# Optimization experiments

Hardware: AMD Instinct MI355X
Metric: run time of the kernel (lower is better)

## Reference

```python
import jax, jax.numpy as jnp
import numpy as np

# dims: batch, tokens, model dim, heads, head_dim, context len, n_blocks, ffn dim
B, L, D, H, HD, S, NB, DFF = 1, 3072, 1024, 16, 64, 512, 2, 4096
T3, H3, W3 = 12, 16, 16  # latent video grid, T3*H3*W3 == L


def _ln(x):
    # LayerNorm, elementwise_affine=False, eps=1e-6
    m = jnp.mean(x, axis=-1, keepdims=True)
    v = jnp.mean(jnp.square(x - m), axis=-1, keepdims=True)
    return (x - m) * jax.lax.rsqrt(v + 1e-6)


def _rot_half(x):
    x1, x2 = jnp.split(x, 2, axis=-1)
    return jnp.concatenate([-x2, x1], axis=-1)


def _rope3d(head_dim, t, h, w):
    d = head_dim // 6
    def band(n):
        freqs = 1.0 / 10000.0 ** (np.arange(0, 2 * d, 2, dtype=np.float32) / (2 * d))
        return np.outer(np.arange(n, dtype=np.float32), freqs)  # [n, d]
    te, he, we = band(t), band(h), band(w)
    rope = np.zeros((t, h, w, head_dim), dtype=np.float32)
    rope[:, :, :, :d] = te[:, None, None, :]
    rope[:, :, :, d:2 * d] = he[None, :, None, :]
    rope[:, :, :, 2 * d:3 * d] = we[None, None, :, :]
    return jnp.asarray(rope.reshape(t * h * w, head_dim))


def _forward(x, timestep_emb, context_emb, rope_emb, adaW, adab, sqW, skW, svW,
             soW, sob, cqW, ckW, cvW, coW, cob, f1W, f1b, f2W, f2b):
    Bv, Lv, Dv = x.shape
    hd = rope_emb.shape[-1]
    nh = Dv // hd
    scale = hd ** -0.5
    cos = jnp.cos(rope_emb)[None, None]  # [1,1,L,hd]
    sin = jnp.sin(rope_emb)[None, None]

    def heads(y):  # [B,N,D] -> [B,H,N,hd]
        return y.reshape(Bv, -1, nh, hd).transpose(0, 2, 1, 3)

    def merge(y):  # [B,H,L,hd] -> [B,L,D]
        return y.transpose(0, 2, 1, 3).reshape(Bv, Lv, Dv)

    for i in range(adaW.shape[0]):
        mods = timestep_emb @ adaW[i].T + adab[i]  # [B, 6D]
        sh_msa, sc_msa, g_msa, sh_mlp, sc_mlp, g_mlp = jnp.split(mods, 6, axis=-1)
        # --- AdaLN + self-attention with RoPE ---
        hx = _ln(x) * (1.0 + sc_msa[:, None, :]) + sh_msa[:, None, :]
        q, k, v = heads(hx @ sqW[i].T), heads(hx @ skW[i].T), heads(hx @ svW[i].T)
        q = q * cos + _rot_half(q) * sin
        k = k * cos + _rot_half(k) * sin
        a = jax.nn.softmax(jnp.einsum('bhld,bhmd->bhlm', q, k) * scale, axis=-1)
        o = merge(jnp.einsum('bhlm,bhmd->bhld', a, v))
        x = x + g_msa[:, None, :] * (o @ soW[i].T + sob[i])
        # --- cross-attention (no gate, no modulation) ---
        hx = _ln(x)
        q = heads(hx @ cqW[i].T)
        k = heads(context_emb @ ckW[i].T)
        v = heads(context_emb @ cvW[i].T)
        a = jax.nn.softmax(jnp.einsum('bhld,bhsd->bhls', q, k) * scale, axis=-1)
        o = merge(jnp.einsum('bhls,bhsd->bhld', a, v))
        x = x + (o @ coW[i].T + cob[i])
        # --- AdaLN + MLP (exact GELU) ---
        hx = _ln(x) * (1.0 + sc_mlp[:, None, :]) + sh_mlp[:, None, :]
        hx = jax.nn.gelu(hx @ f1W[i].T + f1b[i], approximate=False)
        x = x + g_mlp[:, None, :] * (hx @ f2W[i].T + f2b[i])
    return x


def setup_inputs() -> dict:
    ks = jax.random.split(jax.random.key(0), 20)
    s = 0.02
    return {
        'x': jax.random.normal(ks[0], (B, L, D), jnp.float32),
        'timestep_emb': jax.random.normal(ks[1], (B, D), jnp.float32),
        'context_emb': jax.random.normal(ks[2], (B, S, D), jnp.float32),
        'rope_emb': _rope3d(HD, T3, H3, W3),
        'adaW': jax.random.normal(ks[3], (NB, 6 * D, D), jnp.float32) * s,
        'adab': jnp.zeros((NB, 6 * D), jnp.float32),
        'sqW': jax.random.normal(ks[4], (NB, D, D), jnp.float32) * s,
        'skW': jax.random.normal(ks[5], (NB, D, D), jnp.float32) * s,
        'svW': jax.random.normal(ks[6], (NB, D, D), jnp.float32) * s,
        'soW': jax.random.normal(ks[7], (NB, D, D), jnp.float32) * s,
        'sob': jnp.zeros((NB, D), jnp.float32),
        'cqW': jax.random.normal(ks[8], (NB, D, D), jnp.float32) * s,
        'ckW': jax.random.normal(ks[9], (NB, D, D), jnp.float32) * s,
        'cvW': jax.random.normal(ks[10], (NB, D, D), jnp.float32) * s,
        'coW': jax.random.normal(ks[11], (NB, D, D), jnp.float32) * s,
        'cob': jnp.zeros((NB, D), jnp.float32),
        'f1W': jax.random.normal(ks[12], (NB, DFF, D), jnp.float32) * s,
        'f1b': jnp.zeros((NB, DFF), jnp.float32),
        'f2W': jax.random.normal(ks[13], (NB, D, DFF), jnp.float32) * s,
        'f2b': jnp.zeros((NB, D), jnp.float32),
    }


def reference(x, timestep_emb, context_emb, rope_emb, adaW, adab, sqW, skW, svW,
              soW, sob, cqW, ckW, cvW, coW, cob, f1W, f1b, f2W, f2b):
    return _forward(x, timestep_emb, context_emb, rope_emb, adaW, adab, sqW, skW,
                    svW, soW, sob, cqW, ckW, cvW, coW, cob, f1W, f1b, f2W, f2b)
```

## Files before the change

kernel.cpp:

```cpp
#include <hip/hip_runtime.h>
#include <math.h>

typedef __attribute__((ext_vector_type(8))) short bf16x8;
typedef __attribute__((ext_vector_type(4))) float f32x4;
typedef unsigned short u16;
typedef unsigned int u32;

#define DEV static __device__ __forceinline__

typedef __attribute__((address_space(3))) u32 lds_u32;
typedef const __attribute__((address_space(1))) u32 glb_u32;

DEV void gload16(const void* g, void* l){
  __builtin_amdgcn_global_load_lds((glb_u32*)g, (lds_u32*)l, 16, 0, 0);
}

DEV u16 f2bf(float f){
  u32 u = __builtin_bit_cast(u32, f);
  u32 r = (u + 0x7fffu + ((u >> 16) & 1u)) >> 16;
  return (u16)r;
}
DEV float bf2f(u16 h){
  u32 u = ((u32)h) << 16;
  return __builtin_bit_cast(float, u);
}
DEV u32 pack2(float a, float b){
  u32 ua = (__builtin_bit_cast(u32, a) + 0x8000u) >> 16;
  u32 ub = (__builtin_bit_cast(u32, b) + 0x8000u) & 0xffff0000u;
  return ua | ub;
}
DEV float gelu_exact(float x){ return 0.5f*x*(1.f+erff(x*0.70710678118654752f)); }

DEV void xcd_remap(int &bx, int &by){
  int gx = gridDim.x, gy = gridDim.y;
  int n = gx*gy;
  if ((n & 7) == 0){
    int id = by*gx + bx;
    int q = n >> 3;
    int sid = (id & 7)*q + (id >> 3);
    bx = sid % gx;
    by = sid / gx;
  }
}

__global__ __launch_bounds__(256) void k_copy_f32(const float* __restrict__ in, float* __restrict__ out, int n4){
  int i = blockIdx.x*256 + threadIdx.x;
  if (i < n4) ((float4*)out)[i] = ((const float4*)in)[i];
}

__global__ __launch_bounds__(256) void k_cvt_bf16(const float* __restrict__ in, u16* __restrict__ out, int n4){
  int i = blockIdx.x*256 + threadIdx.x;
  if (i < n4){
    float4 v = ((const float4*)in)[i];
    ushort4 o;
    o.x = f2bf(v.x); o.y = f2bf(v.y); o.z = f2bf(v.z); o.w = f2bf(v.w);
    ((ushort4*)out)[i] = o;
  }
}

__global__ __launch_bounds__(256) void k_ada(const float* __restrict__ te,
    const float* __restrict__ adaW, const float* __restrict__ adab,
    float* __restrict__ mods){
  int row = blockIdx.x*4 + (threadIdx.x>>6);
  int lane = threadIdx.x & 63;
  const float* wr = adaW + (size_t)row*1024;
  float s = 0.f;
  #pragma unroll
  for (int j=0; j<4; j++){
    int c = lane*4 + j*256;
    float4 a = *(const float4*)(te + c);
    float4 b = *(const float4*)(wr + c);
    s += a.x*b.x + a.y*b.y + a.z*b.z + a.w*b.w;
  }
  #pragma unroll
  for (int off=32; off; off>>=1) s += __shfl_down(s, off);
  if (!lane) mods[row] = s + adab[row];
}

__global__ __launch_bounds__(256) void k_ln_mod(const float* __restrict__ x,
    const float* __restrict__ sh, const float* __restrict__ sc,
    u16* __restrict__ out){
  int row = blockIdx.x, t = threadIdx.x;
  const float* xr = x + (size_t)row*1024;
  float4 v = ((const float4*)xr)[t];
  float s  = v.x+v.y+v.z+v.w;
  float sq = v.x*v.x+v.y*v.y+v.z*v.z+v.w*v.w;
  #pragma unroll
  for (int off=32; off; off>>=1){ s += __shfl_down(s,off); sq += __shfl_down(sq,off); }
  __shared__ float red[8];
  int w = t>>6, lane = t&63;
  if (!lane){ red[w] = s; red[4+w] = sq; }
  __syncthreads();
  s  = red[0]+red[1]+red[2]+red[3];
  sq = red[4]+red[5]+red[6]+red[7];
  float mean = s*(1.f/1024.f);
  float var  = sq*(1.f/1024.f) - mean*mean;
  float rst  = rsqrtf(var + 1e-6f);
  float vv[4] = {v.x, v.y, v.z, v.w};
  ushort4 o;
  u16 ob[4];
  #pragma unroll
  for (int j=0;j<4;j++){
    int col = t*4+j;
    float y = (vv[j]-mean)*rst;
    if (sh) y = y*(1.f + sc[col]) + sh[col];
    ob[j] = f2bf(y);
  }
  o.x=ob[0]; o.y=ob[1]; o.z=ob[2]; o.w=ob[3];
  *(ushort4*)(out + (size_t)row*1024 + t*4) = o;
}

__global__ __launch_bounds__(256) void k_rope(u16* __restrict__ q, u16* __restrict__ k,
    const float* __restrict__ rope){
  int idx = blockIdx.x*256 + threadIdx.x;
  int d = idx & 31;
  int h = (idx >> 5) & 15;
  int p = idx >> 9;
  const float* rr = rope + (size_t)p*64;
  float a0 = rr[d], a1 = rr[d+32];
  float c0 = cosf(a0), s0 = sinf(a0);
  float c1 = cosf(a1), s1 = sinf(a1);
  size_t o = (size_t)p*1024 + h*64 + d;
  float q0 = bf2f(q[o]), q1 = bf2f(q[o+32]);
  q[o]    = f2bf((q0*c0 - q1*s0)*0.125f);
  q[o+32] = f2bf((q1*c1 + q0*s1)*0.125f);
  float k0 = bf2f(k[o]), k1 = bf2f(k[o+32]);
  k[o]    = f2bf(k0*c0 - k1*s0);
  k[o+32] = f2bf(k1*c1 + k0*s1);
}

DEV void gemm_loop(const u16* __restrict__ X, const u16* __restrict__ W,
                   int bm, int bn, int K, u16* As, u16* Bs, f32x4 acc[4][4])
{
  int t = threadIdx.x;
  int w = t>>6, lane = t&63;
  int wr = (w>>1)*64, wc = (w&1)*64;
  int fr = lane&15, g = lane>>4;
  int arow = lane>>2, acol = (lane&3)*8;
  const u16* xp = X + (size_t)(bm + w*32 + arow)*K + acol;
  const u16* wp = W + (size_t)(bn + w*32 + arow)*K + acol;
  int nk = K >> 5;
  {
    u16* a = As + w*1024; u16* b = Bs + w*1024;
    gload16(xp, a);             gload16(xp + (size_t)16*K, a + 512);
    gload16(wp, b);             gload16(wp + (size_t)16*K, b + 512);
  }
  for (int kt = 0; kt < nk; ++kt){
    __syncthreads();
    int cur = kt & 1;
    if (kt + 1 < nk){
      int nb = cur ^ 1;
      int k0 = (kt+1) << 5;
      u16* a = As + nb*4096 + w*1024; u16* b = Bs + nb*4096 + w*1024;
      gload16(xp + k0, a);        gload16(xp + k0 + (size_t)16*K, a + 512);
      gload16(wp + k0, b);        gload16(wp + k0 + (size_t)16*K, b + 512);
    }
    const u16* ab = As + cur*4096;
    const u16* bb = Bs + cur*4096;
    bf16x8 a[4], b[4];
    #pragma unroll
    for (int i=0;i<4;i++) a[i] = *(const bf16x8*)(ab + (wr+i*16+fr)*32 + g*8);
    #pragma unroll
    for (int i=0;i<4;i++) b[i] = *(const bf16x8*)(bb + (wc+i*16+fr)*32 + g*8);
    #pragma unroll
    for (int i=0;i<4;i++)
      #pragma unroll
      for (int j=0;j<4;j++)
        acc[i][j] = __builtin_amdgcn_mfma_f32_16x16x32_bf16(a[i], b[j], acc[i][j], 0, 0, 0);
  }
}

template<int EPI>
__global__ __launch_bounds__(256) void k_gemm_bf16(
    const u16* __restrict__ X, const u16* __restrict__ W,
    const float* __restrict__ bias,
    u16* __restrict__ Yout,
    const float* __restrict__ resin, float* __restrict__ resout,
    const float* __restrict__ gate,
    int M, int N, int K)
{
  __shared__ __align__(16) u16 As[2*128*32];
  __shared__ __align__(16) u16 Bs[2*128*32];
  int bx = blockIdx.x, by = blockIdx.y;
  xcd_remap(bx, by);
  int bm = bx*128, bn = by*128;
  f32x4 acc[4][4] = {};
  gemm_loop(X, W, bm, bn, K, As, Bs, acc);
  int lane = threadIdx.x & 63, w = threadIdx.x>>6;
  int wr = (w>>1)*64, wc = (w&1)*64;
  int fr = lane&15, g = lane>>4;
  #pragma unroll
  for (int i=0;i<4;i++){
    #pragma unroll
    for (int j=0;j<4;j++){
      int col = bn + wc + j*16 + fr;
      float bv = bias ? bias[col] : 0.f;
      #pragma unroll
      for (int r=0;r<4;r++){
        int row = bm + wr + i*16 + g*4 + r;
        float y = acc[i][j][r] + bv;
        if (EPI == 1){
          Yout[(size_t)row*N + col] = f2bf(gelu_exact(y));
        } else if (EPI == 2){
          float gt = gate ? gate[col] : 1.f;
          resout[(size_t)row*N + col] = resin[(size_t)row*N + col] + gt*y;
        } else {
          Yout[(size_t)row*N + col] = f2bf(y*0.125f);
        }
      }
    }
  }
}

template<int MODE>
__global__ __launch_bounds__(256) void k_qkv(
    const u16* __restrict__ X,
    const u16* __restrict__ W0, const u16* __restrict__ W1, const u16* __restrict__ W2,
    u16* __restrict__ Y0, u16* __restrict__ Y1, u16* __restrict__ VT,
    int M, int ldvt)
{
  __shared__ __align__(16) u16 As[2*128*32];
  __shared__ __align__(16) u16 Bs[2*128*32];
  int bx = blockIdx.x, by = blockIdx.y;
  xcd_remap(bx, by);
  int bm = bx*128, bn = by*128;
  int sel = bn >> 10;
  int bnl = bn & 1023;
  const u16* W = (MODE==0) ? (sel==0 ? W0 : (sel==1 ? W1 : W2))
                           : (sel==0 ? W0 : W1);
  f32x4 acc[4][4] = {};
  {
    gemm_loop(X, W, bm, bnl, 1024, As, Bs, acc);
  }
  int lane = threadIdx.x & 63, w = threadIdx.x>>6;
  int wr = (w>>1)*64, wc = (w&1)*64;
  int fr = lane&15, g = lane>>4;
  const int lastSel = (MODE==0) ? 2 : 1;
  if (sel < lastSel){
    u16* Y = (sel==0) ? Y0 : Y1;
    #pragma unroll
    for (int i=0;i<4;i++)
      #pragma unroll
      for (int j=0;j<4;j++){
        int col = bnl + wc + j*16 + fr;
        #pragma unroll
        for (int r=0;r<4;r++){
          int row = bm + wr + i*16 + g*4 + r;
          Y[(size_t)row*1024 + col] = f2bf(acc[i][j][r]);
        }
      }
  } else {
    #pragma unroll
    for (int i=0;i<4;i++)
      #pragma unroll
      for (int j=0;j<4;j++){
        int col = bnl + wc + j*16 + fr;
        int row0 = bm + wr + i*16 + g*4;
        uint2 pk;
        pk.x = pack2(acc[i][j][0], acc[i][j][1]);
        pk.y = pack2(acc[i][j][2], acc[i][j][3]);
        *(uint2*)(VT + (size_t)col*ldvt + row0) = pk;
      }
  }
}

template<int EPI>
__global__ __launch_bounds__(256) void k_gemm_f32(
    const u16* __restrict__ X, const float* __restrict__ W,
    const float* __restrict__ bias,
    u16* __restrict__ Yout,
    const float* __restrict__ resin, float* __restrict__ resout,
    const float* __restrict__ gate,
    int M, int N, int K)
{
  __shared__ __align__(16) u16 As[128][32];
  __shared__ __align__(16) u16 Bs[128][40];
  int bx = blockIdx.x, by = blockIdx.y;
  xcd_remap(bx, by);
  int bm = bx*128, bn = by*128;
  int t = threadIdx.x;
  int w = t>>6, lane = t&63;
  int wr = (w>>1)*64, wc = (w&1)*64;
  int fr = lane&15, g = lane>>4;
  f32x4 acc[4][4] = {};
  int arow = lane>>2, acol = (lane&3)*8;
  int srow = t>>2, scol = (t&3)*8;
  for (int k0=0; k0<K; k0+=32){
    #pragma unroll
    for (int inst=0; inst<2; ++inst){
      int r = w*32 + inst*16 + arow;
      gload16(X + (size_t)(bm+r)*K + k0 + acol, &As[w*32+inst*16][0]);
    }
    #pragma unroll
    for (int it=0; it<2; ++it){
      const float* wp = W + (size_t)(bn+srow+it*64)*K + k0 + scol;
      float4 f0 = *(const float4*)(wp);
      float4 f1 = *(const float4*)(wp+4);
      uint4 bw;
      bw.x = (u32)f2bf(f0.x) | ((u32)f2bf(f0.y)<<16);
      bw.y = (u32)f2bf(f0.z) | ((u32)f2bf(f0.w)<<16);
      bw.z = (u32)f2bf(f1.x) | ((u32)f2bf(f1.y)<<16);
      bw.w = (u32)f2bf(f1.z) | ((u32)f2bf(f1.w)<<16);
      *(uint4*)&Bs[srow+it*64][scol] = bw;
    }
    __syncthreads();
    bf16x8 a[4], b[4];
    #pragma unroll
    for (int i=0;i<4;i++) a[i] = *(const bf16x8*)&As[wr+i*16+fr][g*8];
    #pragma unroll
    for (int i=0;i<4;i++) b[i] = *(const bf16x8*)&Bs[wc+i*16+fr][g*8];
    #pragma unroll
    for (int i=0;i<4;i++)
      #pragma unroll
      for (int j=0;j<4;j++)
        acc[i][j] = __builtin_amdgcn_mfma_f32_16x16x32_bf16(a[i], b[j], acc[i][j], 0, 0, 0);
    __syncthreads();
  }
  #pragma unroll
  for (int i=0;i<4;i++){
    #pragma unroll
    for (int j=0;j<4;j++){
      int col = bn + wc + j*16 + fr;
      float bv = bias ? bias[col] : 0.f;
      #pragma unroll
      for (int r=0;r<4;r++){
        int row = bm + wr + i*16 + g*4 + r;
        float y = acc[i][j][r] + bv;
        if (EPI == 0){
          Yout[(size_t)row*N + col] = f2bf(y);
        } else if (EPI == 1){
          Yout[(size_t)row*N + col] = f2bf(gelu_exact(y));
        } else if (EPI == 2){
          float gt = gate ? gate[col] : 1.f;
          resout[(size_t)row*N + col] = resin[(size_t)row*N + col] + gt*y;
        } else if (EPI == 3){
          Yout[(size_t)col*M + row] = f2bf(y);
        } else {
          Yout[(size_t)row*N + col] = f2bf(y*0.125f);
        }
      }
    }
  }
}

__global__ __launch_bounds__(256) void k_flash(
    const u16* __restrict__ Q, const u16* __restrict__ Kb, const u16* __restrict__ VT,
    u16* __restrict__ O, int Lkv)
{
  __shared__ __align__(16) u16 Ks[2*64*64];
  __shared__ __align__(16) u16 Vs[2*64*64];
  __shared__ __align__(16) u16 Ps[4][16][72];
  int bx = blockIdx.x, by = blockIdx.y;
  xcd_remap(bx, by);
  int h = by;
  int q0 = bx*64;
  int t = threadIdx.x, w = t>>6, lane = t&63;
  int fr = lane&15, g = lane>>4;
  const u16* qrow = Q + (size_t)(q0 + w*16 + fr)*1024 + h*64;
  bf16x8 aq0 = *(const bf16x8*)(qrow + g*8);
  bf16x8 aq1 = *(const bf16x8*)(qrow + 32 + g*8);
  f32x4 accO[4] = {};
  float m = -1e30f, l = 0.f;
  int slot = lane & 7, rop = lane >> 3;
  const u16* kbase = Kb + (size_t)h*64;
  const u16* vbase = VT + (size_t)h*64*Lkv;
  int nt = Lkv >> 6;
  {
    #pragma unroll
    for (int inst=0; inst<2; ++inst){
      int row = w*16 + inst*8 + rop;
      int ss = slot ^ (row & 7);
      gload16(kbase + (size_t)row*1024 + ss*8, Ks + (w*16+inst*8)*64);
      gload16(vbase + (size_t)row*Lkv + ss*8, Vs + (w*16+inst*8)*64);
    }
  }
  for (int tt=0; tt<nt; ++tt){
    __syncthreads();
    int cur = tt & 1;
    if (tt+1 < nt){
      int nb = cur ^ 1;
      int k0 = (tt+1) << 6;
      #pragma unroll
      for (int inst=0; inst<2; ++inst){
        int row = w*16 + inst*8 + rop;
        int ss = slot ^ (row & 7);
        gload16(kbase + (size_t)(k0+row)*1024 + ss*8, Ks + nb*4096 + (w*16+inst*8)*64);
        gload16(vbase + (size_t)row*Lkv + k0 + ss*8, Vs + nb*4096 + (w*16+inst*8)*64);
      }
    }
    const u16* kc = Ks + cur*4096;
    const u16* vc = Vs + cur*4096;
    f32x4 st[4] = {};
    #pragma unroll
    for (int kb=0;kb<4;kb++){
      int rowK = kb*16 + fr;
      bf16x8 b0 = *(const bf16x8*)(kc + rowK*64 + ((g  ) ^ (rowK&7))*8);
      bf16x8 b1 = *(const bf16x8*)(kc + rowK*64 + ((4+g) ^ (rowK&7))*8);
      st[kb] = __builtin_amdgcn_mfma_f32_16x16x32_bf16(b0, aq0, st[kb], 0,0,0);
      st[kb] = __builtin_amdgcn_mfma_f32_16x16x32_bf16(b1, aq1, st[kb], 0,0,0);
    }
    float x[16];
    #pragma unroll
    for (int kb=0;kb<4;kb++)
      #pragma unroll
      for (int r=0;r<4;r++) x[kb*4+r] = st[kb][r];
    float tmax = x[0];
    #pragma unroll
    for (int ii=1; ii<16; ii++) tmax = fmaxf(tmax, x[ii]);
    tmax = fmaxf(tmax, __shfl_xor(tmax, 16));
    tmax = fmaxf(tmax, __shfl_xor(tmax, 32));
    if (!__all(tmax <= m + 8.f)){
      float mn = fmaxf(m, tmax);
      float er = __expf(m - mn);
      m = mn;
      l *= er;
      #pragma unroll
      for (int r=0;r<4;r++){
        float erq = __shfl(er, g*4+r);
        #pragma unroll
        for (int nd=0; nd<4; nd++) accO[nd][r] *= erq;
      }
    }
    float ts = 0.f;
    u32 pk[8];
    #pragma unroll
    for (int kb=0;kb<4;kb++){
      float p0 = __expf(x[kb*4+0] - m);
      float p1 = __expf(x[kb*4+1] - m);
      float p2 = __expf(x[kb*4+2] - m);
      float p3 = __expf(x[kb*4+3] - m);
      ts += (p0+p1)+(p2+p3);
      pk[kb*2]   = pack2(p0,p1);
      pk[kb*2+1] = pack2(p2,p3);
    }
    ts += __shfl_xor(ts, 16);
    ts += __shfl_xor(ts, 32);
    l += ts;
    #pragma unroll
    for (int kb=0;kb<4;kb++){
      uint2 pv; pv.x = pk[kb*2]; pv.y = pk[kb*2+1];
      *(uint2*)&Ps[w][fr][kb*16 + g*4] = pv;
    }
    bf16x8 ap0 = *(const bf16x8*)&Ps[w][fr][g*8];
    bf16x8 ap1 = *(const bf16x8*)&Ps[w][fr][32 + g*8];
    #pragma unroll
    for (int nd=0; nd<4; nd++){
      int rowV = nd*16 + fr;
      bf16x8 b0 = *(const bf16x8*)(vc + rowV*64 + ((g  ) ^ (rowV&7))*8);
      bf16x8 b1 = *(const bf16x8*)(vc + rowV*64 + ((4+g) ^ (rowV&7))*8);
      accO[nd] = __builtin_amdgcn_mfma_f32_16x16x32_bf16(ap0, b0, accO[nd], 0,0,0);
      accO[nd] = __builtin_amdgcn_mfma_f32_16x16x32_bf16(ap1, b1, accO[nd], 0,0,0);
    }
  }
  float rl = 1.f / l;
  #pragma unroll
  for (int r=0;r<4;r++){
    float rlq = __shfl(rl, g*4+r);
    int row = q0 + w*16 + g*4 + r;
    #pragma unroll
    for (int nd=0; nd<4; nd++)
      O[(size_t)row*1024 + h*64 + nd*16 + fr] = f2bf(accO[nd][r] * rlq);
  }
}

extern "C" void kernel_launch(void* const* d_in, const int* in_sizes, int n_in,
                              void* d_out, int out_size, void* d_ws, size_t ws_size,
                              hipStream_t stream){
  const float* x_in = (const float*)d_in[0];
  const float* te   = (const float*)d_in[1];
  const float* ctx  = (const float*)d_in[2];
  const float* rope = (const float*)d_in[3];
  const float* adaW = (const float*)d_in[4];
  const float* adab = (const float*)d_in[5];
  const float* sqW  = (const float*)d_in[6];
  const float* skW  = (const float*)d_in[7];
  const float* svW  = (const float*)d_in[8];
  const float* soW  = (const float*)d_in[9];
  const float* sob  = (const float*)d_in[10];
  const float* cqW  = (const float*)d_in[11];
  const float* ckW  = (const float*)d_in[12];
  const float* cvW  = (const float*)d_in[13];
  const float* coW  = (const float*)d_in[14];
  const float* cob  = (const float*)d_in[15];
  const float* f1W  = (const float*)d_in[16];
  const float* f1b  = (const float*)d_in[17];
  const float* f2W  = (const float*)d_in[18];
  const float* f2b  = (const float*)d_in[19];
  float* x = (float*)d_out;

  char* p = (char*)d_ws;
  size_t used = 0;
  auto alloc = [&](size_t bytes){
    void* r = (void*)(p + used);
    used += (bytes + 255) & ~(size_t)255;
    return r;
  };
  u16* hx   = (u16*)alloc((size_t)3072*1024*2);
  u16* qb   = (u16*)alloc((size_t)3072*1024*2);
  u16* kb   = (u16*)alloc((size_t)3072*1024*2);
  u16* vt   = (u16*)alloc((size_t)1024*3072*2);
  u16* ob   = (u16*)alloc((size_t)3072*1024*2);
  u16* mid  = (u16*)alloc((size_t)3072*4096*2);
  u16* ctxb = (u16*)alloc((size_t)512*1024*2);
  float* mods = (float*)alloc((size_t)2*6144*4);
  size_t base_used = used;
  const size_t NW_SMALL = (size_t)2*1024*1024;
  const size_t NW_BIG   = (size_t)2*4096*1024;
  size_t wbytes = (8*NW_SMALL + 2*NW_BIG)*2;
  bool pre = (base_used + wbytes + 4096) <= ws_size;

  u16 *sqWb=nullptr,*skWb=nullptr,*svWb=nullptr,*soWb=nullptr,
      *cqWb=nullptr,*ckWb=nullptr,*cvWb=nullptr,*coWb=nullptr,
      *f1Wb=nullptr,*f2Wb=nullptr;
  if (pre){
    sqWb=(u16*)alloc(NW_SMALL*2); skWb=(u16*)alloc(NW_SMALL*2);
    svWb=(u16*)alloc(NW_SMALL*2); soWb=(u16*)alloc(NW_SMALL*2);
    cqWb=(u16*)alloc(NW_SMALL*2); ckWb=(u16*)alloc(NW_SMALL*2);
    cvWb=(u16*)alloc(NW_SMALL*2); coWb=(u16*)alloc(NW_SMALL*2);
    f1Wb=(u16*)alloc(NW_BIG*2);   f2Wb=(u16*)alloc(NW_BIG*2);
    auto CVT = [&](const float* s, u16* d, size_t n){
      k_cvt_bf16<<<(int)(n/1024), 256, 0, stream>>>(s, d, (int)(n/4));
    };
    CVT(sqW,sqWb,NW_SMALL); CVT(skW,skWb,NW_SMALL);
    CVT(svW,svWb,NW_SMALL); CVT(soW,soWb,NW_SMALL);
    CVT(cqW,cqWb,NW_SMALL); CVT(ckW,ckWb,NW_SMALL);
    CVT(cvW,cvWb,NW_SMALL); CVT(coW,coWb,NW_SMALL);
    CVT(f1W,f1Wb,NW_BIG);   CVT(f2W,f2Wb,NW_BIG);
  }

  k_copy_f32<<<3072, 256, 0, stream>>>(x_in, x, 786432);
  k_cvt_bf16<<<512, 256, 0, stream>>>(ctx, ctxb, 131072);
  k_ada<<<3072, 256, 0, stream>>>(te, adaW, adab, mods);

  for (int i=0; i<2; ++i){
    const float* mi = mods + (size_t)i*6144;
    size_t wo = (size_t)i*1024*1024;
    size_t wof = (size_t)i*4096*1024;
    k_ln_mod<<<3072,256,0,stream>>>(x, mi+0, mi+1024, hx);
    if (pre){
      k_qkv<0><<<dim3(24,24),256,0,stream>>>(hx, sqWb+wo, skWb+wo, svWb+wo, qb, kb, vt, 3072, 3072);
    } else {
      k_gemm_f32<0><<<dim3(24,8),256,0,stream>>>(hx, sqW+wo, nullptr, qb, nullptr,nullptr,nullptr, 3072,1024,1024);
      k_gemm_f32<0><<<dim3(24,8),256,0,stream>>>(hx, skW+wo, nullptr, kb, nullptr,nullptr,nullptr, 3072,1024,1024);
      k_gemm_f32<3><<<dim3(24,8),256,0,stream>>>(hx, svW+wo, nullptr, vt, nullptr,nullptr,nullptr, 3072,1024,1024);
    }
    k_rope<<<6144,256,0,stream>>>(qb, kb, rope);
    k_flash<<<dim3(48,16),256,0,stream>>>(qb, kb, vt, ob, 3072);
    if (pre)
      k_gemm_bf16<2><<<dim3(24,8),256,0,stream>>>(ob, soWb+wo, sob+(size_t)i*1024, nullptr, x, x, mi+2048, 3072,1024,1024);
    else
      k_gemm_f32<2><<<dim3(24,8),256,0,stream>>>(ob, soW+wo, sob+(size_t)i*1024, nullptr, x, x, mi+2048, 3072,1024,1024);
    k_ln_mod<<<3072,256,0,stream>>>(x, nullptr, nullptr, hx);
    if (pre){
      k_gemm_bf16<4><<<dim3(24,8),256,0,stream>>>(hx, cqWb+wo, nullptr, qb, nullptr,nullptr,nullptr, 3072,1024,1024);
      k_qkv<1><<<dim3(4,16),256,0,stream>>>(ctxb, ckWb+wo, cvWb+wo, nullptr, kb, nullptr, vt, 512, 512);
    } else {
      k_gemm_f32<4><<<dim3(24,8),256,0,stream>>>(hx, cqW+wo, nullptr, qb, nullptr,nullptr,nullptr, 3072,1024,1024);
      k_gemm_f32<0><<<dim3(4,8),256,0,stream>>>(ctxb, ckW+wo, nullptr, kb, nullptr,nullptr,nullptr, 512,1024,1024);
      k_gemm_f32<3><<<dim3(4,8),256,0,stream>>>(ctxb, cvW+wo, nullptr, vt, nullptr,nullptr,nullptr, 512,1024,1024);
    }
    k_flash<<<dim3(48,16),256,0,stream>>>(qb, kb, vt, ob, 512);
    if (pre)
      k_gemm_bf16<2><<<dim3(24,8),256,0,stream>>>(ob, coWb+wo, cob+(size_t)i*1024, nullptr, x, x, nullptr, 3072,1024,1024);
    else
      k_gemm_f32<2><<<dim3(24,8),256,0,stream>>>(ob, coW+wo, cob+(size_t)i*1024, nullptr, x, x, nullptr, 3072,1024,1024);
    k_ln_mod<<<3072,256,0,stream>>>(x, mi+3072, mi+4096, hx);
    if (pre){
      k_gemm_bf16<1><<<dim3(24,32),256,0,stream>>>(hx, f1Wb+wof, f1b+(size_t)i*4096, mid, nullptr,nullptr,nullptr, 3072,4096,1024);
      k_gemm_bf16<2><<<dim3(24,8),256,0,stream>>>(mid, f2Wb+wof, f2b+(size_t)i*1024, nullptr, x, x, mi+5120, 3072,1024,4096);
    } else {
      k_gemm_f32<1><<<dim3(24,32),256,0,stream>>>(hx, f1W+wof, f1b+(size_t)i*4096, mid, nullptr,nullptr,nullptr, 3072,4096,1024);
      k_gemm_f32<2><<<dim3(24,8),256,0,stream>>>(mid, f2W+wof, f2b+(size_t)i*1024, nullptr, x, x, mi+5120, 3072,1024,4096);
    }
  }
}
```

Before: 948.1 us.

## Deepen GEMM and flash-attention LDS pipelines to four stages with swizzle

Both the shared GEMM loop and the flash attention kernel move from double-buffered LDS staging to a 4-buffer ring with three tiles prefetched ahead. The per-iteration __syncthreads becomes an explicit vmcnt wait plus s_barrier, so earlier loads can stay in flight while the current tile is consumed. The GEMM LDS layout gains an XOR swizzle on the column chunk to cut bank conflicts, and MFMA sections are wrapped in s_setprio. The cost is double the LDS footprint per block, which may lower occupancy. The hand-written vmcnt counts also assume each wave has exactly four outstanding loads per stage.

```diff
diff --git a/kernel.cpp b/kernel.cpp
--- a/kernel.cpp
+++ b/kernel.cpp
@@ -130,43 +130,52 @@
 }
 
 DEV void gemm_loop(const u16* __restrict__ X, const u16* __restrict__ W,
-                   int bm, int bn, int K, u16* As, u16* Bs, f32x4 acc[4][4])
+                   int bm, int bn, int ld, int lenK, u16* As, u16* Bs, f32x4 acc[4][4])
 {
   int t = threadIdx.x;
   int w = t>>6, lane = t&63;
   int wr = (w>>1)*64, wc = (w&1)*64;
   int fr = lane&15, g = lane>>4;
-  int arow = lane>>2, acol = (lane&3)*8;
-  const u16* xp = X + (size_t)(bm + w*32 + arow)*K + acol;
-  const u16* wp = W + (size_t)(bn + w*32 + arow)*K + acol;
-  int nk = K >> 5;
-  {
-    u16* a = As + w*1024; u16* b = Bs + w*1024;
-    gload16(xp, a);             gload16(xp + (size_t)16*K, a + 512);
-    gload16(wp, b);             gload16(wp + (size_t)16*K, b + 512);
-  }
+  int arow = lane>>2;
+  int acol = ((lane&3) ^ (arow&3))*8;
+  const u16* xp = X + (size_t)(bm + w*32 + arow)*ld + acol;
+  const u16* wp = W + (size_t)(bn + w*32 + arow)*ld + acol;
+  int nk = lenK >> 5;
+  auto stage = [&](int kt){
+    int buf = kt & 3;
+    int k0 = kt << 5;
+    u16* a = As + buf*4096 + w*1024;
+    u16* b = Bs + buf*4096 + w*1024;
+    gload16(xp + k0, a);  gload16(xp + k0 + (size_t)16*ld, a + 512);
+    gload16(wp + k0, b);  gload16(wp + k0 + (size_t)16*ld, b + 512);
+  };
+  stage(0); stage(1); stage(2);
   for (int kt = 0; kt < nk; ++kt){
-    __syncthreads();
-    int cur = kt & 1;
-    if (kt + 1 < nk){
-      int nb = cur ^ 1;
-      int k0 = (kt+1) << 5;
-      u16* a = As + nb*4096 + w*1024; u16* b = Bs + nb*4096 + w*1024;
-      gload16(xp + k0, a);        gload16(xp + k0 + (size_t)16*K, a + 512);
-      gload16(wp + k0, b);        gload16(wp + k0 + (size_t)16*K, b + 512);
-    }
-    const u16* ab = As + cur*4096;
-    const u16* bb = Bs + cur*4096;
+    int rem = nk - 1 - kt;
+    if (rem >= 2)      asm volatile("s_waitcnt vmcnt(8)\n\ts_barrier" ::: "memory");
+    else if (rem == 1) asm volatile("s_waitcnt vmcnt(4)\n\ts_barrier" ::: "memory");
+    else               asm volatile("s_waitcnt vmcnt(0)\n\ts_barrier" ::: "memory");
+    if (kt + 3 < nk) stage(kt+3);
+    const u16* ab = As + (kt&3)*4096;
+    const u16* bb = Bs + (kt&3)*4096;
     bf16x8 a[4], b[4];
     #pragma unroll
-    for (int i=0;i<4;i++) a[i] = *(const bf16x8*)(ab + (wr+i*16+fr)*32 + g*8);
-    #pragma unroll
-    for (int i=0;i<4;i++) b[i] = *(const bf16x8*)(bb + (wc+i*16+fr)*32 + g*8);
+    for (int i=0;i<4;i++){
+      int row = wr+i*16+fr;
+      a[i] = *(const bf16x8*)(ab + row*32 + ((g ^ (fr&3))*8));
+    }
+    #pragma unroll
+    for (int i=0;i<4;i++){
+      int row = wc+i*16+fr;
+      b[i] = *(const bf16x8*)(bb + row*32 + ((g ^ (fr&3))*8));
+    }
+    __builtin_amdgcn_s_setprio(1);
     #pragma unroll
     for (int i=0;i<4;i++)
       #pragma unroll
       for (int j=0;j<4;j++)
         acc[i][j] = __builtin_amdgcn_mfma_f32_16x16x32_bf16(a[i], b[j], acc[i][j], 0, 0, 0);
+    __builtin_amdgcn_s_setprio(0);
   }
 }
 
@@ -179,13 +188,13 @@
     const float* __restrict__ gate,
     int M, int N, int K)
 {
-  __shared__ __align__(16) u16 As[2*128*32];
-  __shared__ __align__(16) u16 Bs[2*128*32];
+  __shared__ __align__(16) u16 As[4*128*32];
+  __shared__ __align__(16) u16 Bs[4*128*32];
   int bx = blockIdx.x, by = blockIdx.y;
   xcd_remap(bx, by);
   int bm = bx*128, bn = by*128;
   f32x4 acc[4][4] = {};
-  gemm_loop(X, W, bm, bn, K, As, Bs, acc);
+  gemm_loop(X, W, bm, bn, K, K, As, Bs, acc);
   int lane = threadIdx.x & 63, w = threadIdx.x>>6;
   int wr = (w>>1)*64, wc = (w&1)*64;
   int fr = lane&15, g = lane>>4;
@@ -219,8 +228,8 @@
     u16* __restrict__ Y0, u16* __restrict__ Y1, u16* __restrict__ VT,
     int M, int ldvt)
 {
-  __shared__ __align__(16) u16 As[2*128*32];
-  __shared__ __align__(16) u16 Bs[2*128*32];
+  __shared__ __align__(16) u16 As[4*128*32];
+  __shared__ __align__(16) u16 Bs[4*128*32];
   int bx = blockIdx.x, by = blockIdx.y;
   xcd_remap(bx, by);
   int bm = bx*128, bn = by*128;
@@ -229,9 +238,7 @@
   const u16* W = (MODE==0) ? (sel==0 ? W0 : (sel==1 ? W1 : W2))
                            : (sel==0 ? W0 : W1);
   f32x4 acc[4][4] = {};
-  {
-    gemm_loop(X, W, bm, bnl, 1024, As, Bs, acc);
-  }
+  gemm_loop(X, W, bm, bnl, 1024, 1024, As, Bs, acc);
   int lane = threadIdx.x & 63, w = threadIdx.x>>6;
   int wr = (w>>1)*64, wc = (w&1)*64;
   int fr = lane&15, g = lane>>4;
@@ -347,8 +354,8 @@
     const u16* __restrict__ Q, const u16* __restrict__ Kb, const u16* __restrict__ VT,
     u16* __restrict__ O, int Lkv)
 {
-  __shared__ __align__(16) u16 Ks[2*64*64];
-  __shared__ __align__(16) u16 Vs[2*64*64];
+  __shared__ __align__(16) u16 Ks[4*64*64];
+  __shared__ __align__(16) u16 Vs[4*64*64];
   __shared__ __align__(16) u16 Ps[4][16][72];
   int bx = blockIdx.x, by = blockIdx.y;
   xcd_remap(bx, by);
@@ -359,38 +366,35 @@
   const u16* qrow = Q + (size_t)(q0 + w*16 + fr)*1024 + h*64;
   bf16x8 aq0 = *(const bf16x8*)(qrow + g*8);
   bf16x8 aq1 = *(const bf16x8*)(qrow + 32 + g*8);
+  asm volatile("s_waitcnt vmcnt(0)" ::: "memory");
   f32x4 accO[4] = {};
   float m = -1e30f, l = 0.f;
   int slot = lane & 7, rop = lane >> 3;
   const u16* kbase = Kb + (size_t)h*64;
   const u16* vbase = VT + (size_t)h*64*Lkv;
   int nt = Lkv >> 6;
-  {
+  auto stage = [&](int tt){
+    int buf = tt & 3;
+    int k0 = tt << 6;
     #pragma unroll
     for (int inst=0; inst<2; ++inst){
       int row = w*16 + inst*8 + rop;
       int ss = slot ^ (row & 7);
-      gload16(kbase + (size_t)row*1024 + ss*8, Ks + (w*16+inst*8)*64);
-      gload16(vbase + (size_t)row*Lkv + ss*8, Vs + (w*16+inst*8)*64);
-    }
-  }
+      gload16(kbase + (size_t)(k0+row)*1024 + ss*8, Ks + buf*4096 + (w*16+inst*8)*64);
+      gload16(vbase + (size_t)row*Lkv + k0 + ss*8, Vs + buf*4096 + (w*16+inst*8)*64);
+    }
+  };
+  stage(0); stage(1); stage(2);
   for (int tt=0; tt<nt; ++tt){
-    __syncthreads();
-    int cur = tt & 1;
-    if (tt+1 < nt){
-      int nb = cur ^ 1;
-      int k0 = (tt+1) << 6;
-      #pragma unroll
-      for (int inst=0; inst<2; ++inst){
-        int row = w*16 + inst*8 + rop;
-        int ss = slot ^ (row & 7);
-        gload16(kbase + (size_t)(k0+row)*1024 + ss*8, Ks + nb*4096 + (w*16+inst*8)*64);
-        gload16(vbase + (size_t)row*Lkv + k0 + ss*8, Vs + nb*4096 + (w*16+inst*8)*64);
-      }
-    }
-    const u16* kc = Ks + cur*4096;
-    const u16* vc = Vs + cur*4096;
+    int rem = nt - 1 - tt;
+    if (rem >= 2)      asm volatile("s_waitcnt vmcnt(8)\n\ts_barrier" ::: "memory");
+    else if (rem == 1) asm volatile("s_waitcnt vmcnt(4)\n\ts_barrier" ::: "memory");
+    else               asm volatile("s_waitcnt vmcnt(0)\n\ts_barrier" ::: "memory");
+    if (tt + 3 < nt) stage(tt+3);
+    const u16* kc = Ks + (tt&3)*4096;
+    const u16* vc = Vs + (tt&3)*4096;
     f32x4 st[4] = {};
+    __builtin_amdgcn_s_setprio(1);
     #pragma unroll
     for (int kb=0;kb<4;kb++){
       int rowK = kb*16 + fr;
@@ -399,6 +403,7 @@
       st[kb] = __builtin_amdgcn_mfma_f32_16x16x32_bf16(b0, aq0, st[kb], 0,0,0);
       st[kb] = __builtin_amdgcn_mfma_f32_16x16x32_bf16(b1, aq1, st[kb], 0,0,0);
     }
+    __builtin_amdgcn_s_setprio(0);
     float x[16];
     #pragma unroll
     for (int kb=0;kb<4;kb++)
@@ -443,6 +448,7 @@
     }
     bf16x8 ap0 = *(const bf16x8*)&Ps[w][fr][g*8];
     bf16x8 ap1 = *(const bf16x8*)&Ps[w][fr][32 + g*8];
+    __builtin_amdgcn_s_setprio(1);
     #pragma unroll
     for (int nd=0; nd<4; nd++){
       int rowV = nd*16 + fr;
@@ -451,6 +457,7 @@
       accO[nd] = __builtin_amdgcn_mfma_f32_16x16x32_bf16(ap0, b0, accO[nd], 0,0,0);
       accO[nd] = __builtin_amdgcn_mfma_f32_16x16x32_bf16(ap1, b1, accO[nd], 0,0,0);
     }
+    __builtin_amdgcn_s_setprio(0);
   }
   float rl = 1.f / l;
   #pragma unroll
```

New measurement: 1.116 ms. +17.7%, slower.
